# Kernel optimization log

Measured on AMD Instinct MI355X. Metric: run time of the kernel, lower is better.

Reference implementation:

```python
import jax, jax.numpy as jnp
import numpy as np

T, B, A = 128, 512, 5
X, Y, Z, H, R = 2, 10, 32, 128, 128
LOG2PI = np.float32(np.log(2.0 * np.pi))


def setup_inputs() -> dict:
    key = jax.random.key(0)
    ks = iter(jax.random.split(key, 40))
    w = lambda *s: jax.random.normal(next(ks), s, jnp.float32) * 0.05
    return dict(
        states=jax.random.normal(next(ks), (T, B, Y), jnp.float32),
        eps=jax.random.normal(next(ks), (T - 1, B, A, Z), jnp.float32),
        enc_w1=w(A, X + Y + R, H), enc_b1=w(A, H),
        enc_w2=w(A, H, H), enc_b2=w(A, H),
        enc_mw=w(A, H, Z), enc_mb=w(A, Z),
        enc_sw=w(A, H, Z), enc_sb=w(A, Z),
        pri_w1=w(A, Y + R, H), pri_b1=w(A, H),
        pri_w2=w(A, H, H), pri_b2=w(A, H),
        pri_mw=w(A, H, Z), pri_mb=w(A, Z),
        pri_sw=w(A, H, Z), pri_sb=w(A, Z),
        dec_w1=w(A, Y + Z + R, H), dec_b1=w(A, H),
        dec_w2=w(A, H, H), dec_b2=w(A, H),
        dec_mw=w(A, H, X), dec_mb=w(A, X),
        dec_sw=w(A, H, X), dec_sb=w(A, X),
        gru_wih=w(A, X + Z, 3 * R), gru_whh=w(A, R, 3 * R),
        gru_bih=w(A, 3 * R), gru_bhh=w(A, 3 * R),
    )


def _lin(x, wt, b):
    # x: [B, A, I], wt: [A, I, O] -> [B, A, O]  (per-agent linear)
    return jnp.einsum('bai,aio->bao', x, wt) + b


def _mlp(x, w1, b1, w2, b2):
    return jax.nn.relu(_lin(jax.nn.relu(_lin(x, w1, b1)), w2, b2))


def reference(states, eps, enc_w1, enc_b1, enc_w2, enc_b2, enc_mw, enc_mb,
              enc_sw, enc_sb, pri_w1, pri_b1, pri_w2, pri_b2, pri_mw, pri_mb,
              pri_sw, pri_sb, dec_w1, dec_b1, dec_w2, dec_b2, dec_mw, dec_mb,
              dec_sw, dec_sb, gru_wih, gru_whh, gru_bih, gru_bhh):
    y_all = states[:-1]                              # [T-1, B, Y]
    x_all = states[1:].reshape(T - 1, B, A, X)       # per-agent next positions

    def step(carry, xs):
        h, kl, nll = carry                           # h: [B, A, R]
        y, x, e = xs                                 # y:[B,Y] x:[B,A,X] e:[B,A,Z]
        yb = jnp.broadcast_to(y[:, None, :], (B, A, Y))
        enc_h = _mlp(jnp.concatenate([x, yb, h], -1), enc_w1, enc_b1, enc_w2, enc_b2)
        enc_m = _lin(enc_h, enc_mw, enc_mb)
        enc_s = jax.nn.softplus(_lin(enc_h, enc_sw, enc_sb))
        pri_h = _mlp(jnp.concatenate([yb, h], -1), pri_w1, pri_b1, pri_w2, pri_b2)
        pri_m = _lin(pri_h, pri_mw, pri_mb)
        pri_s = jax.nn.softplus(_lin(pri_h, pri_sw, pri_sb))
        z = enc_m + enc_s * e                         # reparameterized sample
        dec_h = _mlp(jnp.concatenate([yb, z, h], -1), dec_w1, dec_b1, dec_w2, dec_b2)
        dec_m = _lin(dec_h, dec_mw, dec_mb)
        dec_s = jax.nn.softplus(_lin(dec_h, dec_sw, dec_sb))
        # GRU cell (torch gate order: r, z, n)
        gi = _lin(jnp.concatenate([x, z], -1), gru_wih, gru_bih)   # [B,A,3R]
        gh = _lin(h, gru_whh, gru_bhh)
        gir, giz, gin = jnp.split(gi, 3, -1)
        ghr, ghz, ghn = jnp.split(gh, 3, -1)
        r = jax.nn.sigmoid(gir + ghr)
        u = jax.nn.sigmoid(giz + ghz)
        n = jnp.tanh(gin + r * ghn)
        h_new = (1.0 - u) * n + u * h
        kl_t = 0.5 * jnp.sum(2.0 * jnp.log(pri_s) - 2.0 * jnp.log(enc_s)
                             + (enc_s ** 2 + (enc_m - pri_m) ** 2) / pri_s ** 2 - 1.0)
        nll_t = jnp.sum(0.5 * LOG2PI + jnp.log(dec_s) + 0.5 * ((x - dec_m) / dec_s) ** 2)
        return (h_new, kl + kl_t, nll + nll_t), None

    h0 = jnp.zeros((B, A, R), states.dtype)
    zero = jnp.zeros((), states.dtype)
    (h, kl, nll), _ = jax.lax.scan(step, (h0, zero, zero), (y_all, x_all, eps))
    return jnp.stack([kl, nll])  # [kl_loss, recon_loss]
```

## Files before the change

kernel.cpp:

```cpp
#include <hip/hip_runtime.h>

typedef __attribute__((ext_vector_type(8))) short bf16x8;
typedef __attribute__((ext_vector_type(4))) float f32x4;

#define MFMA_B16(A,B,C) __builtin_amdgcn_mfma_f32_16x16x32_bf16((A),(B),(C),0,0,0)

#define FO_ENC1 0
#define FO_PRI1 48
#define FO_DEC1 88
#define FO_GIH  136
#define FO_GHH  184
#define FO_ENC2 280
#define FO_PRI2 312
#define FO_DEC2 344
#define FO_MS   376
#define FO_DECMS 408
#define NFRAG   412

#define MS 200
#define TS 136

__device__ __forceinline__ unsigned short f2bf(float f) {
  union { float f; unsigned u; } v; v.f = f;
  unsigned r = (v.u + 0x7fffu + ((v.u >> 16) & 1u)) >> 16;
  return (unsigned short)r;
}
__device__ __forceinline__ float bf2f(unsigned short h) {
  union { unsigned u; float f; } v; v.u = ((unsigned)h) << 16;
  return v.f;
}
__device__ __forceinline__ float sigm_(float x) { return 1.f / (1.f + __expf(-x)); }
__device__ __forceinline__ float tanh_(float x) {
  x = fminf(fmaxf(x, -15.f), 15.f);
  float e = __expf(-2.f * x);
  return (1.f - e) / (1.f + e);
}
__device__ __forceinline__ float splus_(float x) {
  return fmaxf(x, 0.f) + log1pf(__expf(-fabsf(x)));
}
__device__ __forceinline__ float ldnt(const float* p) {
  return __builtin_nontemporal_load(p);
}

__global__ void prep_kernel(const float* __restrict__ ew1, const float* __restrict__ pw1,
                            const float* __restrict__ dw1, const float* __restrict__ wih,
                            const float* __restrict__ whh, const float* __restrict__ ew2,
                            const float* __restrict__ pw2, const float* __restrict__ dw2,
                            const float* __restrict__ emw, const float* __restrict__ esw,
                            const float* __restrict__ pmw, const float* __restrict__ psw,
                            const float* __restrict__ dmw, const float* __restrict__ dsw,
                            unsigned short* __restrict__ ws)
{
  int blk = blockIdx.x;
  int a = blk / NFRAG, f = blk % NFRAG;
  int l = threadIdx.x, lg = l >> 4, ln = l & 15;
  float v[8];

  if (f < FO_PRI1) {
    int fi = f, nt = fi / 6, kb = fi % 6, n = nt * 16 + ln;
#pragma unroll
    for (int j = 0; j < 8; ++j) {
      int mk = kb * 32 + lg * 8 + j;
      int r = (mk < 2) ? mk : (mk >= 34 && mk < 44) ? 2 + (mk - 34)
            : (mk >= 64) ? 12 + (mk - 64) : -1;
      v[j] = (r >= 0) ? ew1[((size_t)a * 140 + r) * 128 + n] : 0.f;
    }
  } else if (f < FO_DEC1) {
    int fi = f - FO_PRI1, nt = fi / 5, kb = 1 + fi % 5, n = nt * 16 + ln;
#pragma unroll
    for (int j = 0; j < 8; ++j) {
      int mk = kb * 32 + lg * 8 + j;
      int r = (mk >= 34 && mk < 44) ? (mk - 34) : (mk >= 64) ? 10 + (mk - 64) : -1;
      v[j] = (r >= 0) ? pw1[((size_t)a * 138 + r) * 128 + n] : 0.f;
    }
  } else if (f < FO_GIH) {
    int fi = f - FO_DEC1, nt = fi / 6, kb = fi % 6, n = nt * 16 + ln;
#pragma unroll
    for (int j = 0; j < 8; ++j) {
      int mk = kb * 32 + lg * 8 + j;
      int r = (mk >= 2 && mk < 34) ? 10 + (mk - 2) : (mk >= 34 && mk < 44) ? (mk - 34)
            : (mk >= 64) ? 42 + (mk - 64) : -1;
      v[j] = (r >= 0) ? dw1[((size_t)a * 170 + r) * 128 + n] : 0.f;
    }
  } else if (f < FO_GHH) {
    int fi = f - FO_GIH, nt = fi / 2, kb = fi % 2, n = nt * 16 + ln;
#pragma unroll
    for (int j = 0; j < 8; ++j) {
      int mk = kb * 32 + lg * 8 + j;
      v[j] = (mk < 34) ? wih[((size_t)a * 34 + mk) * 384 + n] : 0.f;
    }
  } else if (f < FO_ENC2) {
    int fi = f - FO_GHH, nt = fi / 4, kb = fi % 4, n = nt * 16 + ln;
#pragma unroll
    for (int j = 0; j < 8; ++j) {
      int r = kb * 32 + lg * 8 + j;
      v[j] = whh[((size_t)a * 128 + r) * 384 + n];
    }
  } else if (f < FO_DEC2) {
    int fi = f - FO_ENC2;
    const float* W = (fi < 32) ? ew2 : pw2;
    fi &= 31;
    int nt = fi / 4, kb = fi % 4, n = nt * 16 + ln;
#pragma unroll
    for (int j = 0; j < 8; ++j) {
      int r = kb * 32 + lg * 8 + j;
      v[j] = W[((size_t)a * 128 + r) * 128 + n];
    }
  } else if (f < FO_MS) {
    int fi = f - FO_DEC2, nt = fi / 4, kb = fi % 4, n = nt * 16 + ln;
#pragma unroll
    for (int j = 0; j < 8; ++j) {
      int r = kb * 32 + lg * 8 + j;
      v[j] = dw2[((size_t)a * 128 + r) * 128 + n];
    }
  } else if (f < FO_DECMS) {
    int fi = f - FO_MS, mat = fi / 8, rem = fi % 8, nt = rem / 4, kb = rem % 4;
    int n = nt * 16 + ln;
    const float* W = (mat == 0) ? emw : (mat == 1) ? esw : (mat == 2) ? pmw : psw;
#pragma unroll
    for (int j = 0; j < 8; ++j) {
      int r = kb * 32 + lg * 8 + j;
      v[j] = W[((size_t)a * 128 + r) * 32 + n];
    }
  } else {
    int kb = f - FO_DECMS;
#pragma unroll
    for (int j = 0; j < 8; ++j) {
      int r = kb * 32 + lg * 8 + j;
      v[j] = (ln < 2) ? dmw[((size_t)a * 128 + r) * 2 + ln]
           : (ln < 4) ? dsw[((size_t)a * 128 + r) * 2 + (ln - 2)] : 0.f;
    }
  }
  unsigned short* dst = ws + (size_t)blk * 512 + l * 8;
#pragma unroll
  for (int j = 0; j < 8; ++j) dst[j] = f2bf(v[j]);
}

#define LD_FRAG(idx) (*(const bf16x8*)(fa + (size_t)(idx) * 512 + l * 8))

__global__ __launch_bounds__(256, 1) void vrnn_main(
    const float* __restrict__ states, const float* __restrict__ eps,
    const float* __restrict__ eb1, const float* __restrict__ eb2,
    const float* __restrict__ emb, const float* __restrict__ esb,
    const float* __restrict__ pb1, const float* __restrict__ pb2,
    const float* __restrict__ pmb, const float* __restrict__ psb,
    const float* __restrict__ db1, const float* __restrict__ db2,
    const float* __restrict__ dmb, const float* __restrict__ dsb,
    const float* __restrict__ bih, const float* __restrict__ bhh,
    const unsigned short* __restrict__ frags, float* __restrict__ out)
{
  const int a = blockIdx.y;
  const int b0 = blockIdx.x * 16;
  const int tid = threadIdx.x;
  const int w = tid >> 6, l = tid & 63, lg = l >> 4, ln = l & 15;

  __shared__ __align__(16) unsigned short ghh_lds[96 * 512];
  __shared__ __align__(16) unsigned short ms_lds[32 * 512];
  __shared__ __align__(16) unsigned short dms_lds[4 * 512];
  __shared__ __align__(16) unsigned short master[16 * MS];
  __shared__ __align__(16) unsigned short t1e[16 * TS], t1p[16 * TS];
  __shared__ __align__(16) unsigned short he[16 * TS], hp[16 * TS];
  __shared__ float msbuf[2][16][32];
  __shared__ float red[8];

  const unsigned short* fa = frags + (size_t)a * NFRAG * 512;

  {
    const uint4* s1 = (const uint4*)(fa + (size_t)FO_GHH * 512);
    uint4* d1 = (uint4*)ghh_lds;
    for (int i = tid; i < 96 * 64; i += 256) d1[i] = s1[i];
    const uint4* s2 = (const uint4*)(fa + (size_t)FO_MS * 512);
    uint4* d2 = (uint4*)ms_lds;
    for (int i = tid; i < 32 * 64; i += 256) d2[i] = s2[i];
    const uint4* s3 = (const uint4*)(fa + (size_t)FO_DECMS * 512);
    uint4* d3 = (uint4*)dms_lds;
    d3[tid] = s3[tid];
  }
  for (int i = tid; i < 16 * MS; i += 256) master[i] = 0;

  float eb1v[2], pb1v[2], eb2v[2], pb2v[2], db2v[2], d1b[2], ghb[3][2];
#pragma unroll
  for (int j = 0; j < 2; ++j) {
    int n = (w + 4 * j) * 16 + ln;
    eb1v[j] = eb1[a * 128 + n]; pb1v[j] = pb1[a * 128 + n];
    eb2v[j] = eb2[a * 128 + n]; pb2v[j] = pb2[a * 128 + n];
    db2v[j] = db2[a * 128 + n]; d1b[j]  = db1[a * 128 + n];
#pragma unroll
    for (int g = 0; g < 3; ++g)
      ghb[g][j] = bih[a * 384 + g * 128 + n] + bhh[a * 384 + g * 128 + n];
  }
  float hbm, hbs, dmsb = 0.f;
  if (w < 2) { hbm = emb[a * 32 + w * 16 + ln]; hbs = esb[a * 32 + w * 16 + ln]; }
  else { hbm = pmb[a * 32 + (w - 2) * 16 + ln]; hbs = psb[a * 32 + (w - 2) * 16 + ln]; }
  if (w == 0) dmsb = (ln < 2) ? dmb[a * 2 + ln] : (ln < 4) ? dsb[a * 2 + (ln - 2)] : 0.f;

  __syncthreads();

  if (tid < 160) {
    int row = tid / 10, c = tid - row * 10;
    master[row * MS + 34 + c] = f2bf(ldnt(states + (size_t)b0 * 10 + tid));
  }
  if (tid >= 192 && tid < 224) {
    int i = tid - 192, row = i >> 1, c = i & 1;
    master[row * MS + c] = f2bf(ldnt(states + ((size_t)512 + b0 + row) * 10 + a * 2 + c));
  }
  float e_cur[4] = {0.f, 0.f, 0.f, 0.f};
  if (w < 2) {
#pragma unroll
    for (int q = 0; q < 4; ++q)
      e_cur[q] = ldnt(eps + ((size_t)(b0 + 4 * lg + q) * 5 + a) * 32 + w * 16 + ln);
  }
  float xv[4] = {0.f, 0.f, 0.f, 0.f};
  float kl = 0.f, nll = 0.f;
  f32x4 em = {0, 0, 0, 0}, esv = {0, 0, 0, 0};
  f32x4 gh[3][2];
  float hn[8];
  __syncthreads();

  for (int t = 0; t < 127; ++t) {
    if (w == 0 && t > 0) {
      f32x4 acc = {dmsb, dmsb, dmsb, dmsb};
#pragma unroll
      for (int kb = 0; kb < 4; ++kb) {
        bf16x8 ad = *(const bf16x8*)&he[ln * TS + kb * 32 + lg * 8];
        bf16x8 bf = *(const bf16x8*)&dms_lds[kb * 512 + l * 8];
        acc = MFMA_B16(ad, bf, acc);
      }
#pragma unroll
      for (int q = 0; q < 4; ++q) {
        float sv = __shfl(splus_(acc[q]), l + 2);
        if (ln < 2) {
          float d = (xv[q] - acc[q]) / sv;
          nll += 0.9189385332f + __logf(sv) + 0.5f * d * d;
        }
      }
    }
    {
      bf16x8 f1[12], f2[10];
#pragma unroll
      for (int j = 0; j < 2; ++j) {
#pragma unroll
        for (int kb = 0; kb < 6; ++kb) f1[j * 6 + kb] = LD_FRAG(FO_ENC1 + (w + 4 * j) * 6 + kb);
#pragma unroll
        for (int kb = 0; kb < 5; ++kb) f2[j * 5 + kb] = LD_FRAG(FO_PRI1 + (w + 4 * j) * 5 + kb);
      }
      bf16x8 am[6];
#pragma unroll
      for (int kb = 0; kb < 6; ++kb)
        am[kb] = *(const bf16x8*)&master[ln * MS + kb * 32 + lg * 8];
#pragma unroll
      for (int j = 0; j < 2; ++j) {
        f32x4 a1 = {eb1v[j], eb1v[j], eb1v[j], eb1v[j]};
        f32x4 a2 = {pb1v[j], pb1v[j], pb1v[j], pb1v[j]};
#pragma unroll
        for (int kb = 0; kb < 6; ++kb) a1 = MFMA_B16(am[kb], f1[j * 6 + kb], a1);
#pragma unroll
        for (int kb = 0; kb < 5; ++kb) a2 = MFMA_B16(am[kb + 1], f2[j * 5 + kb], a2);
#pragma unroll
        for (int q = 0; q < 4; ++q) {
          t1e[(4 * lg + q) * TS + (w + 4 * j) * 16 + ln] = f2bf(fmaxf(a1[q], 0.f));
          t1p[(4 * lg + q) * TS + (w + 4 * j) * 16 + ln] = f2bf(fmaxf(a2[q], 0.f));
        }
      }
    }
    __syncthreads();

    {
      bf16x8 g1[8], g2[8];
#pragma unroll
      for (int j = 0; j < 2; ++j)
#pragma unroll
        for (int kb = 0; kb < 4; ++kb) {
          g1[j * 4 + kb] = LD_FRAG(FO_ENC2 + (w + 4 * j) * 4 + kb);
          g2[j * 4 + kb] = LD_FRAG(FO_PRI2 + (w + 4 * j) * 4 + kb);
        }
      bf16x8 ae[4], ap[4];
#pragma unroll
      for (int kb = 0; kb < 4; ++kb) {
        ae[kb] = *(const bf16x8*)&t1e[ln * TS + kb * 32 + lg * 8];
        ap[kb] = *(const bf16x8*)&t1p[ln * TS + kb * 32 + lg * 8];
      }
#pragma unroll
      for (int j = 0; j < 2; ++j) {
        f32x4 a1 = {eb2v[j], eb2v[j], eb2v[j], eb2v[j]};
        f32x4 a2 = {pb2v[j], pb2v[j], pb2v[j], pb2v[j]};
#pragma unroll
        for (int kb = 0; kb < 4; ++kb) {
          a1 = MFMA_B16(ae[kb], g1[j * 4 + kb], a1);
          a2 = MFMA_B16(ap[kb], g2[j * 4 + kb], a2);
        }
#pragma unroll
        for (int q = 0; q < 4; ++q) {
          he[(4 * lg + q) * TS + (w + 4 * j) * 16 + ln] = f2bf(fmaxf(a1[q], 0.f));
          hp[(4 * lg + q) * TS + (w + 4 * j) * 16 + ln] = f2bf(fmaxf(a2[q], 0.f));
        }
      }
    }
    __syncthreads();

    {
      const unsigned short* hs = (w < 2) ? he : hp;
      int mbase = ((w < 2) ? 0 : 16) + (w & 1) * 4;
      bf16x8 ah[4];
#pragma unroll
      for (int kb = 0; kb < 4; ++kb)
        ah[kb] = *(const bf16x8*)&hs[ln * TS + kb * 32 + lg * 8];
      f32x4 m = {hbm, hbm, hbm, hbm}, s = {hbs, hbs, hbs, hbs};
#pragma unroll
      for (int kb = 0; kb < 4; ++kb) {
        m = MFMA_B16(ah[kb], *(const bf16x8*)&ms_lds[(mbase + kb) * 512 + l * 8], m);
        s = MFMA_B16(ah[kb], *(const bf16x8*)&ms_lds[(mbase + 8 + kb) * 512 + l * 8], s);
      }
      if (w < 2) {
        em = m;
#pragma unroll
        for (int q = 0; q < 4; ++q) {
          esv[q] = splus_(s[q]);
          master[(4 * lg + q) * MS + 2 + w * 16 + ln] = f2bf(m[q] + esv[q] * e_cur[q]);
        }
      } else {
#pragma unroll
        for (int q = 0; q < 4; ++q) {
          msbuf[0][4 * lg + q][(w - 2) * 16 + ln] = m[q];
          msbuf[1][4 * lg + q][(w - 2) * 16 + ln] = splus_(s[q]);
        }
      }
      bf16x8 ahh[4];
#pragma unroll
      for (int kb = 0; kb < 4; ++kb)
        ahh[kb] = *(const bf16x8*)&master[ln * MS + (kb + 2) * 32 + lg * 8];
#pragma unroll
      for (int g = 0; g < 3; ++g)
#pragma unroll
        for (int j = 0; j < 2; ++j) {
          float bv = ghb[g][j];
          gh[g][j] = (f32x4){bv, bv, bv, bv};
        }
#pragma unroll
      for (int kb = 0; kb < 4; ++kb)
#pragma unroll
        for (int g = 0; g < 3; ++g)
#pragma unroll
          for (int j = 0; j < 2; ++j)
            gh[g][j] = MFMA_B16(ahh[kb],
              *(const bf16x8*)&ghh_lds[(size_t)((g * 8 + w + 4 * j) * 4 + kb) * 512 + l * 8],
              gh[g][j]);
    }
    __syncthreads();

    {
      if (w < 2 && t < 126) {
#pragma unroll
        for (int q = 0; q < 4; ++q)
          e_cur[q] = ldnt(eps + ((size_t)((t + 1) * 512 + b0 + 4 * lg + q) * 5 + a) * 32
                          + w * 16 + ln);
      }
      if (w == 0) {
#pragma unroll
        for (int q = 0; q < 4; ++q)
          xv[q] = ldnt(states + ((size_t)(t + 1) * 512 + b0 + 4 * lg + q) * 10
                       + a * 2 + (ln & 1));
      }
      bf16x8 fd[12], fg[12];
#pragma unroll
      for (int j = 0; j < 2; ++j)
#pragma unroll
        for (int kb = 0; kb < 6; ++kb)
          fd[j * 6 + kb] = LD_FRAG(FO_DEC1 + (w + 4 * j) * 6 + kb);
#pragma unroll
      for (int g = 0; g < 3; ++g)
#pragma unroll
        for (int j = 0; j < 2; ++j)
#pragma unroll
          for (int kb = 0; kb < 2; ++kb)
            fg[g * 4 + j * 2 + kb] = LD_FRAG(FO_GIH + (g * 8 + w + 4 * j) * 2 + kb);
      bf16x8 am[6];
#pragma unroll
      for (int kb = 0; kb < 6; ++kb)
        am[kb] = *(const bf16x8*)&master[ln * MS + kb * 32 + lg * 8];
#pragma unroll
      for (int j = 0; j < 2; ++j) {
        f32x4 acc = {d1b[j], d1b[j], d1b[j], d1b[j]};
#pragma unroll
        for (int kb = 0; kb < 6; ++kb) acc = MFMA_B16(am[kb], fd[j * 6 + kb], acc);
#pragma unroll
        for (int q = 0; q < 4; ++q)
          t1e[(4 * lg + q) * TS + (w + 4 * j) * 16 + ln] = f2bf(fmaxf(acc[q], 0.f));
      }
      f32x4 gi[3][2];
#pragma unroll
      for (int g = 0; g < 3; ++g)
#pragma unroll
        for (int j = 0; j < 2; ++j) gi[g][j] = (f32x4){0.f, 0.f, 0.f, 0.f};
#pragma unroll
      for (int kb = 0; kb < 2; ++kb)
#pragma unroll
        for (int g = 0; g < 3; ++g)
#pragma unroll
          for (int j = 0; j < 2; ++j)
            gi[g][j] = MFMA_B16(am[kb], fg[g * 4 + j * 2 + kb], gi[g][j]);
#pragma unroll
      for (int j = 0; j < 2; ++j)
#pragma unroll
        for (int q = 0; q < 4; ++q) {
          float r_ = sigm_(gi[0][j][q] + gh[0][j][q]);
          float u_ = sigm_(gi[1][j][q] + gh[1][j][q]);
          float n_ = tanh_(gi[2][j][q] + r_ * gh[2][j][q]);
          float ho = bf2f(master[(4 * lg + q) * MS + 64 + (w + 4 * j) * 16 + ln]);
          hn[j * 4 + q] = (1.f - u_) * n_ + u_ * ho;
        }
      if (w < 2) {
#pragma unroll
        for (int q = 0; q < 4; ++q) {
          float pm = msbuf[0][4 * lg + q][w * 16 + ln];
          float ps = msbuf[1][4 * lg + q][w * 16 + ln];
          float dm = em[q] - pm;
          float es2 = esv[q] * esv[q];
          kl += 0.5f * (2.f * __logf(ps) - 2.f * __logf(esv[q]) + (es2 + dm * dm) / (ps * ps) - 1.f);
        }
      }
    }
    __syncthreads();

    {
      bf16x8 fd2[8];
#pragma unroll
      for (int j = 0; j < 2; ++j)
#pragma unroll
        for (int kb = 0; kb < 4; ++kb)
          fd2[j * 4 + kb] = LD_FRAG(FO_DEC2 + (w + 4 * j) * 4 + kb);
      bf16x8 ad[4];
#pragma unroll
      for (int kb = 0; kb < 4; ++kb)
        ad[kb] = *(const bf16x8*)&t1e[ln * TS + kb * 32 + lg * 8];
#pragma unroll
      for (int j = 0; j < 2; ++j) {
        f32x4 acc = {db2v[j], db2v[j], db2v[j], db2v[j]};
#pragma unroll
        for (int kb = 0; kb < 4; ++kb) acc = MFMA_B16(ad[kb], fd2[j * 4 + kb], acc);
#pragma unroll
        for (int q = 0; q < 4; ++q)
          he[(4 * lg + q) * TS + (w + 4 * j) * 16 + ln] = f2bf(fmaxf(acc[q], 0.f));
      }
#pragma unroll
      for (int j = 0; j < 2; ++j)
#pragma unroll
        for (int q = 0; q < 4; ++q)
          master[(4 * lg + q) * MS + 64 + (w + 4 * j) * 16 + ln] = f2bf(hn[j * 4 + q]);
      if (t < 126) {
        if (w >= 1) {
          int i = (w - 1) * 64 + l;
          if (i < 160) {
            int row = i / 10, c = i - row * 10;
            master[row * MS + 34 + c] =
              f2bf(ldnt(states + ((size_t)(t + 1) * 512 + b0) * 10 + i));
          }
        }
        if (w == 0 && l < 32) {
          int row = l >> 1, c = l & 1;
          master[row * MS + c] =
            f2bf(ldnt(states + ((size_t)(t + 2) * 512 + b0 + row) * 10 + a * 2 + c));
        }
      }
    }
    __syncthreads();
  }

  if (w == 0) {
    f32x4 acc = {dmsb, dmsb, dmsb, dmsb};
#pragma unroll
    for (int kb = 0; kb < 4; ++kb) {
      bf16x8 ad = *(const bf16x8*)&he[ln * TS + kb * 32 + lg * 8];
      bf16x8 bf = *(const bf16x8*)&dms_lds[kb * 512 + l * 8];
      acc = MFMA_B16(ad, bf, acc);
    }
#pragma unroll
    for (int q = 0; q < 4; ++q) {
      float sv = __shfl(splus_(acc[q]), l + 2);
      if (ln < 2) {
        float d = (xv[q] - acc[q]) / sv;
        nll += 0.9189385332f + __logf(sv) + 0.5f * d * d;
      }
    }
  }

#pragma unroll
  for (int off = 32; off > 0; off >>= 1) {
    kl += __shfl_down(kl, off);
    nll += __shfl_down(nll, off);
  }
  if (l == 0) { red[w] = kl; red[4 + w] = nll; }
  __syncthreads();
  if (tid == 0) {
    float K = 0.f, N = 0.f;
#pragma unroll
    for (int i = 0; i < 4; ++i) { K += red[i]; N += red[4 + i]; }
    atomicAdd(out, K);
    atomicAdd(out + 1, N);
  }
}

extern "C" void kernel_launch(void* const* d_in, const int* in_sizes, int n_in,
                              void* d_out, int out_size, void* d_ws, size_t ws_size,
                              hipStream_t stream) {
  (void)in_sizes; (void)n_in; (void)out_size; (void)ws_size;
  const float* states = (const float*)d_in[0];
  const float* eps    = (const float*)d_in[1];
  const float* ew1 = (const float*)d_in[2];
  const float* eb1 = (const float*)d_in[3];
  const float* ew2 = (const float*)d_in[4];
  const float* eb2 = (const float*)d_in[5];
  const float* emw = (const float*)d_in[6];
  const float* emb = (const float*)d_in[7];
  const float* esw = (const float*)d_in[8];
  const float* esb = (const float*)d_in[9];
  const float* pw1 = (const float*)d_in[10];
  const float* pb1 = (const float*)d_in[11];
  const float* pw2 = (const float*)d_in[12];
  const float* pb2 = (const float*)d_in[13];
  const float* pmw = (const float*)d_in[14];
  const float* pmb = (const float*)d_in[15];
  const float* psw = (const float*)d_in[16];
  const float* psb = (const float*)d_in[17];
  const float* dw1 = (const float*)d_in[18];
  const float* db1 = (const float*)d_in[19];
  const float* dw2 = (const float*)d_in[20];
  const float* db2 = (const float*)d_in[21];
  const float* dmw = (const float*)d_in[22];
  const float* dmb = (const float*)d_in[23];
  const float* dsw = (const float*)d_in[24];
  const float* dsb = (const float*)d_in[25];
  const float* wih = (const float*)d_in[26];
  const float* whh = (const float*)d_in[27];
  const float* bih = (const float*)d_in[28];
  const float* bhh = (const float*)d_in[29];

  unsigned short* frags = (unsigned short*)d_ws;
  float* out = (float*)d_out;

  hipMemsetAsync(d_out, 0, 2 * sizeof(float), stream);
  prep_kernel<<<dim3(5 * NFRAG), dim3(64), 0, stream>>>(
      ew1, pw1, dw1, wih, whh, ew2, pw2, dw2, emw, esw, pmw, psw, dmw, dsw, frags);
  vrnn_main<<<dim3(32, 5), dim3(256), 0, stream>>>(
      states, eps, eb1, eb2, emb, esb, pb1, pb2, pmb, psb,
      db1, db2, dmb, dsb, bih, bhh, frags, out);
}
```

Measured before the change: 1.013 ms.

## Restructure VRNN step into three barrier phases with deferred decoder layer two

Reorganizes the per-timestep schedule from four barrier-separated phases to three. The decoder second layer and its mean/std head are deferred into the next step's phases, so they overlap with independent encoder/prior work. The GRU hidden-hidden matmul is hoisted into phase two, and the hidden state is kept in fp32 registers. The master input buffer is double-buffered (MS widened) so next-step states can be prefetched earlier, and mean/std head weights now come from global instead of LDS. The costs are more shared memory, extra buffers, and different LDS/global traffic per step.

```diff
diff --git a/kernel.cpp b/kernel.cpp
--- a/kernel.cpp
+++ b/kernel.cpp
@@ -17,7 +17,7 @@
 #define FO_DECMS 408
 #define NFRAG   412
 
-#define MS 200
+#define MS 264
 #define TS 136
 
 __device__ __forceinline__ unsigned short f2bf(float f) {
@@ -155,12 +155,12 @@
   const int w = tid >> 6, l = tid & 63, lg = l >> 4, ln = l & 15;
 
   __shared__ __align__(16) unsigned short ghh_lds[96 * 512];
-  __shared__ __align__(16) unsigned short ms_lds[32 * 512];
   __shared__ __align__(16) unsigned short dms_lds[4 * 512];
   __shared__ __align__(16) unsigned short master[16 * MS];
   __shared__ __align__(16) unsigned short t1e[16 * TS], t1p[16 * TS];
   __shared__ __align__(16) unsigned short he[16 * TS], hp[16 * TS];
-  __shared__ float msbuf[2][16][32];
+  __shared__ __align__(16) unsigned short t1d[16 * TS], hdbuf[16 * TS];
+  __shared__ float msbuf[4][16][32];
   __shared__ float red[8];
 
   const unsigned short* fa = frags + (size_t)a * NFRAG * 512;
@@ -169,9 +169,6 @@
     const uint4* s1 = (const uint4*)(fa + (size_t)FO_GHH * 512);
     uint4* d1 = (uint4*)ghh_lds;
     for (int i = tid; i < 96 * 64; i += 256) d1[i] = s1[i];
-    const uint4* s2 = (const uint4*)(fa + (size_t)FO_MS * 512);
-    uint4* d2 = (uint4*)ms_lds;
-    for (int i = tid; i < 32 * 64; i += 256) d2[i] = s2[i];
     const uint4* s3 = (const uint4*)(fa + (size_t)FO_DECMS * 512);
     uint4* d3 = (uint4*)dms_lds;
     d3[tid] = s3[tid];
@@ -198,7 +195,7 @@
 
   if (tid < 160) {
     int row = tid / 10, c = tid - row * 10;
-    master[row * MS + 34 + c] = f2bf(ldnt(states + (size_t)b0 * 10 + tid));
+    master[row * MS + 34 + c] = f2bf(ldnt(states + (size_t)(b0 + row) * 10 + c));
   }
   if (tid >= 192 && tid < 224) {
     int i = tid - 192, row = i >> 1, c = i & 1;
@@ -211,30 +208,26 @@
       e_cur[q] = ldnt(eps + ((size_t)(b0 + 4 * lg + q) * 5 + a) * 32 + w * 16 + ln);
   }
   float xv[4] = {0.f, 0.f, 0.f, 0.f};
+  float h_reg[2][4];
+#pragma unroll
+  for (int j = 0; j < 2; ++j)
+#pragma unroll
+    for (int q = 0; q < 4; ++q) h_reg[j][q] = 0.f;
   float kl = 0.f, nll = 0.f;
-  f32x4 em = {0, 0, 0, 0}, esv = {0, 0, 0, 0};
   f32x4 gh[3][2];
-  float hn[8];
   __syncthreads();
 
   for (int t = 0; t < 127; ++t) {
-    if (w == 0 && t > 0) {
-      f32x4 acc = {dmsb, dmsb, dmsb, dmsb};
-#pragma unroll
-      for (int kb = 0; kb < 4; ++kb) {
-        bf16x8 ad = *(const bf16x8*)&he[ln * TS + kb * 32 + lg * 8];
-        bf16x8 bf = *(const bf16x8*)&dms_lds[kb * 512 + l * 8];
-        acc = MFMA_B16(ad, bf, acc);
-      }
-#pragma unroll
-      for (int q = 0; q < 4; ++q) {
-        float sv = __shfl(splus_(acc[q]), l + 2);
-        if (ln < 2) {
-          float d = (xv[q] - acc[q]) / sv;
-          nll += 0.9189385332f + __logf(sv) + 0.5f * d * d;
-        }
-      }
-    }
+    const int base_t = (t & 1) * 200;
+    const int base_n = ((t + 1) & 1) * 200;
+
+    bf16x8 amA[2], am_h[4];
+#pragma unroll
+    for (int kb = 0; kb < 2; ++kb)
+      amA[kb] = *(const bf16x8*)&master[ln * MS + base_t + kb * 32 + lg * 8];
+#pragma unroll
+    for (int kb = 0; kb < 4; ++kb)
+      am_h[kb] = *(const bf16x8*)&master[ln * MS + 64 + kb * 32 + lg * 8];
     {
       bf16x8 f1[12], f2[10];
 #pragma unroll
@@ -244,18 +237,16 @@
 #pragma unroll
         for (int kb = 0; kb < 5; ++kb) f2[j * 5 + kb] = LD_FRAG(FO_PRI1 + (w + 4 * j) * 5 + kb);
       }
-      bf16x8 am[6];
-#pragma unroll
-      for (int kb = 0; kb < 6; ++kb)
-        am[kb] = *(const bf16x8*)&master[ln * MS + kb * 32 + lg * 8];
 #pragma unroll
       for (int j = 0; j < 2; ++j) {
         f32x4 a1 = {eb1v[j], eb1v[j], eb1v[j], eb1v[j]};
         f32x4 a2 = {pb1v[j], pb1v[j], pb1v[j], pb1v[j]};
 #pragma unroll
-        for (int kb = 0; kb < 6; ++kb) a1 = MFMA_B16(am[kb], f1[j * 6 + kb], a1);
-#pragma unroll
-        for (int kb = 0; kb < 5; ++kb) a2 = MFMA_B16(am[kb + 1], f2[j * 5 + kb], a2);
+        for (int kb = 0; kb < 6; ++kb)
+          a1 = MFMA_B16(kb < 2 ? amA[kb] : am_h[kb - 2], f1[j * 6 + kb], a1);
+#pragma unroll
+        for (int i = 0; i < 5; ++i)
+          a2 = MFMA_B16(i == 0 ? amA[1] : am_h[i - 1], f2[j * 5 + i], a2);
 #pragma unroll
         for (int q = 0; q < 4; ++q) {
           t1e[(4 * lg + q) * TS + (w + 4 * j) * 16 + ln] = f2bf(fmaxf(a1[q], 0.f));
@@ -295,12 +286,34 @@
           hp[(4 * lg + q) * TS + (w + 4 * j) * 16 + ln] = f2bf(fmaxf(a2[q], 0.f));
         }
       }
+#pragma unroll
+      for (int g = 0; g < 3; ++g)
+#pragma unroll
+        for (int j = 0; j < 2; ++j) {
+          float bv = ghb[g][j];
+          gh[g][j] = (f32x4){bv, bv, bv, bv};
+        }
+#pragma unroll
+      for (int kb = 0; kb < 4; ++kb)
+#pragma unroll
+        for (int g = 0; g < 3; ++g)
+#pragma unroll
+          for (int j = 0; j < 2; ++j)
+            gh[g][j] = MFMA_B16(am_h[kb],
+              *(const bf16x8*)&ghh_lds[(size_t)((g * 8 + w + 4 * j) * 4 + kb) * 512 + l * 8],
+              gh[g][j]);
     }
     __syncthreads();
 
     {
       const unsigned short* hs = (w < 2) ? he : hp;
-      int mbase = ((w < 2) ? 0 : 16) + (w & 1) * 4;
+      int mbase = FO_MS + ((w < 2) ? 0 : 16) + (w & 1) * 4;
+      bf16x8 fm[4], fs[4];
+#pragma unroll
+      for (int kb = 0; kb < 4; ++kb) {
+        fm[kb] = LD_FRAG(mbase + kb);
+        fs[kb] = LD_FRAG(mbase + 8 + kb);
+      }
       bf16x8 ah[4];
 #pragma unroll
       for (int kb = 0; kb < 4; ++kb)
@@ -308,53 +321,65 @@
       f32x4 m = {hbm, hbm, hbm, hbm}, s = {hbs, hbs, hbs, hbs};
 #pragma unroll
       for (int kb = 0; kb < 4; ++kb) {
-        m = MFMA_B16(ah[kb], *(const bf16x8*)&ms_lds[(mbase + kb) * 512 + l * 8], m);
-        s = MFMA_B16(ah[kb], *(const bf16x8*)&ms_lds[(mbase + 8 + kb) * 512 + l * 8], s);
+        m = MFMA_B16(ah[kb], fm[kb], m);
+        s = MFMA_B16(ah[kb], fs[kb], s);
       }
       if (w < 2) {
-        em = m;
 #pragma unroll
         for (int q = 0; q < 4; ++q) {
-          esv[q] = splus_(s[q]);
-          master[(4 * lg + q) * MS + 2 + w * 16 + ln] = f2bf(m[q] + esv[q] * e_cur[q]);
+          float es = splus_(s[q]);
+          msbuf[0][4 * lg + q][w * 16 + ln] = m[q];
+          msbuf[1][4 * lg + q][w * 16 + ln] = es;
+          master[(4 * lg + q) * MS + base_t + 2 + w * 16 + ln] = f2bf(m[q] + es * e_cur[q]);
         }
       } else {
 #pragma unroll
         for (int q = 0; q < 4; ++q) {
-          msbuf[0][4 * lg + q][(w - 2) * 16 + ln] = m[q];
-          msbuf[1][4 * lg + q][(w - 2) * 16 + ln] = splus_(s[q]);
-        }
-      }
-      bf16x8 ahh[4];
-#pragma unroll
-      for (int kb = 0; kb < 4; ++kb)
-        ahh[kb] = *(const bf16x8*)&master[ln * MS + (kb + 2) * 32 + lg * 8];
-#pragma unroll
-      for (int g = 0; g < 3; ++g)
+          msbuf[2][4 * lg + q][(w - 2) * 16 + ln] = m[q];
+          msbuf[3][4 * lg + q][(w - 2) * 16 + ln] = splus_(s[q]);
+        }
+      }
+      if (t > 0) {
+        bf16x8 fd2[8];
+#pragma unroll
+        for (int j = 0; j < 2; ++j)
+#pragma unroll
+          for (int kb = 0; kb < 4; ++kb)
+            fd2[j * 4 + kb] = LD_FRAG(FO_DEC2 + (w + 4 * j) * 4 + kb);
+        bf16x8 ad[4];
+#pragma unroll
+        for (int kb = 0; kb < 4; ++kb)
+          ad[kb] = *(const bf16x8*)&t1d[ln * TS + kb * 32 + lg * 8];
 #pragma unroll
         for (int j = 0; j < 2; ++j) {
-          float bv = ghb[g][j];
-          gh[g][j] = (f32x4){bv, bv, bv, bv};
-        }
-#pragma unroll
-      for (int kb = 0; kb < 4; ++kb)
-#pragma unroll
-        for (int g = 0; g < 3; ++g)
-#pragma unroll
-          for (int j = 0; j < 2; ++j)
-            gh[g][j] = MFMA_B16(ahh[kb],
-              *(const bf16x8*)&ghh_lds[(size_t)((g * 8 + w + 4 * j) * 4 + kb) * 512 + l * 8],
-              gh[g][j]);
+          f32x4 acc = {db2v[j], db2v[j], db2v[j], db2v[j]};
+#pragma unroll
+          for (int kb = 0; kb < 4; ++kb) acc = MFMA_B16(ad[kb], fd2[j * 4 + kb], acc);
+#pragma unroll
+          for (int q = 0; q < 4; ++q)
+            hdbuf[(4 * lg + q) * TS + (w + 4 * j) * 16 + ln] = f2bf(fmaxf(acc[q], 0.f));
+        }
+      }
+      if (t < 126) {
+        if (tid < 160) {
+          int row = tid / 10, c = tid - row * 10;
+          master[row * MS + base_n + 34 + c] =
+            f2bf(ldnt(states + ((size_t)(t + 1) * 512 + b0 + row) * 10 + c));
+        }
+        if (tid >= 192 && tid < 224) {
+          int i = tid - 192, row = i >> 1, c = i & 1;
+          master[row * MS + base_n + c] =
+            f2bf(ldnt(states + ((size_t)(t + 2) * 512 + b0 + row) * 10 + a * 2 + c));
+        }
+      }
     }
     __syncthreads();
 
     {
-      if (w < 2 && t < 126) {
-#pragma unroll
-        for (int q = 0; q < 4; ++q)
-          e_cur[q] = ldnt(eps + ((size_t)((t + 1) * 512 + b0 + 4 * lg + q) * 5 + a) * 32
-                          + w * 16 + ln);
-      }
+      bf16x8 amZ[2];
+#pragma unroll
+      for (int kb = 0; kb < 2; ++kb)
+        amZ[kb] = *(const bf16x8*)&master[ln * MS + base_t + kb * 32 + lg * 8];
       if (w == 0) {
 #pragma unroll
         for (int q = 0; q < 4; ++q)
@@ -374,18 +399,34 @@
 #pragma unroll
           for (int kb = 0; kb < 2; ++kb)
             fg[g * 4 + j * 2 + kb] = LD_FRAG(FO_GIH + (g * 8 + w + 4 * j) * 2 + kb);
-      bf16x8 am[6];
-#pragma unroll
-      for (int kb = 0; kb < 6; ++kb)
-        am[kb] = *(const bf16x8*)&master[ln * MS + kb * 32 + lg * 8];
+
+      if (w == 0 && t > 0) {
+        f32x4 acc = {dmsb, dmsb, dmsb, dmsb};
+#pragma unroll
+        for (int kb = 0; kb < 4; ++kb) {
+          bf16x8 ad = *(const bf16x8*)&hdbuf[ln * TS + kb * 32 + lg * 8];
+          bf16x8 bf = *(const bf16x8*)&dms_lds[kb * 512 + l * 8];
+          acc = MFMA_B16(ad, bf, acc);
+        }
+#pragma unroll
+        for (int q = 0; q < 4; ++q) {
+          float sv = __shfl(splus_(acc[q]), l + 2);
+          if (ln < 2) {
+            float d = (xv[q] - acc[q]) / sv;
+            nll += 0.9189385332f + __logf(sv) + 0.5f * d * d;
+          }
+        }
+      }
+
 #pragma unroll
       for (int j = 0; j < 2; ++j) {
         f32x4 acc = {d1b[j], d1b[j], d1b[j], d1b[j]};
 #pragma unroll
-        for (int kb = 0; kb < 6; ++kb) acc = MFMA_B16(am[kb], fd[j * 6 + kb], acc);
+        for (int kb = 0; kb < 6; ++kb)
+          acc = MFMA_B16(kb < 2 ? amZ[kb] : am_h[kb - 2], fd[j * 6 + kb], acc);
 #pragma unroll
         for (int q = 0; q < 4; ++q)
-          t1e[(4 * lg + q) * TS + (w + 4 * j) * 16 + ln] = f2bf(fmaxf(acc[q], 0.f));
+          t1d[(4 * lg + q) * TS + (w + 4 * j) * 16 + ln] = f2bf(fmaxf(acc[q], 0.f));
       }
       f32x4 gi[3][2];
 #pragma unroll
@@ -398,7 +439,7 @@
         for (int g = 0; g < 3; ++g)
 #pragma unroll
           for (int j = 0; j < 2; ++j)
-            gi[g][j] = MFMA_B16(am[kb], fg[g * 4 + j * 2 + kb], gi[g][j]);
+            gi[g][j] = MFMA_B16(amZ[kb], fg[g * 4 + j * 2 + kb], gi[g][j]);
 #pragma unroll
       for (int j = 0; j < 2; ++j)
 #pragma unroll
@@ -406,71 +447,57 @@
           float r_ = sigm_(gi[0][j][q] + gh[0][j][q]);
           float u_ = sigm_(gi[1][j][q] + gh[1][j][q]);
           float n_ = tanh_(gi[2][j][q] + r_ * gh[2][j][q]);
-          float ho = bf2f(master[(4 * lg + q) * MS + 64 + (w + 4 * j) * 16 + ln]);
-          hn[j * 4 + q] = (1.f - u_) * n_ + u_ * ho;
-        }
-      if (w < 2) {
-#pragma unroll
-        for (int q = 0; q < 4; ++q) {
-          float pm = msbuf[0][4 * lg + q][w * 16 + ln];
-          float ps = msbuf[1][4 * lg + q][w * 16 + ln];
-          float dm = em[q] - pm;
-          float es2 = esv[q] * esv[q];
-          kl += 0.5f * (2.f * __logf(ps) - 2.f * __logf(esv[q]) + (es2 + dm * dm) / (ps * ps) - 1.f);
-        }
+          float hn = (1.f - u_) * n_ + u_ * h_reg[j][q];
+          h_reg[j][q] = hn;
+          master[(4 * lg + q) * MS + 64 + (w + 4 * j) * 16 + ln] = f2bf(hn);
+        }
+#pragma unroll
+      for (int rr = 0; rr < 2; ++rr) {
+        int elem = rr * 64 + l;
+        int row = w * 4 + (elem >> 5), col = elem & 31;
+        float em_ = msbuf[0][row][col], es_ = msbuf[1][row][col];
+        float pm_ = msbuf[2][row][col], ps_ = msbuf[3][row][col];
+        float dm = em_ - pm_;
+        kl += 0.5f * (2.f * __logf(ps_) - 2.f * __logf(es_)
+                      + (es_ * es_ + dm * dm) / (ps_ * ps_) - 1.f);
+      }
+      if (w < 2 && t < 126) {
+#pragma unroll
+        for (int q = 0; q < 4; ++q)
+          e_cur[q] = ldnt(eps + ((size_t)((t + 1) * 512 + b0 + 4 * lg + q) * 5 + a) * 32
+                          + w * 16 + ln);
       }
     }
     __syncthreads();
-
-    {
-      bf16x8 fd2[8];
-#pragma unroll
-      for (int j = 0; j < 2; ++j)
-#pragma unroll
-        for (int kb = 0; kb < 4; ++kb)
-          fd2[j * 4 + kb] = LD_FRAG(FO_DEC2 + (w + 4 * j) * 4 + kb);
-      bf16x8 ad[4];
+  }
+
+  {
+    bf16x8 fd2[8];
+#pragma unroll
+    for (int j = 0; j < 2; ++j)
 #pragma unroll
       for (int kb = 0; kb < 4; ++kb)
-        ad[kb] = *(const bf16x8*)&t1e[ln * TS + kb * 32 + lg * 8];
-#pragma unroll
-      for (int j = 0; j < 2; ++j) {
-        f32x4 acc = {db2v[j], db2v[j], db2v[j], db2v[j]};
-#pragma unroll
-        for (int kb = 0; kb < 4; ++kb) acc = MFMA_B16(ad[kb], fd2[j * 4 + kb], acc);
-#pragma unroll
-        for (int q = 0; q < 4; ++q)
-          he[(4 * lg + q) * TS + (w + 4 * j) * 16 + ln] = f2bf(fmaxf(acc[q], 0.f));
-      }
-#pragma unroll
-      for (int j = 0; j < 2; ++j)
-#pragma unroll
-        for (int q = 0; q < 4; ++q)
-          master[(4 * lg + q) * MS + 64 + (w + 4 * j) * 16 + ln] = f2bf(hn[j * 4 + q]);
-      if (t < 126) {
-        if (w >= 1) {
-          int i = (w - 1) * 64 + l;
-          if (i < 160) {
-            int row = i / 10, c = i - row * 10;
-            master[row * MS + 34 + c] =
-              f2bf(ldnt(states + ((size_t)(t + 1) * 512 + b0) * 10 + i));
-          }
-        }
-        if (w == 0 && l < 32) {
-          int row = l >> 1, c = l & 1;
-          master[row * MS + c] =
-            f2bf(ldnt(states + ((size_t)(t + 2) * 512 + b0 + row) * 10 + a * 2 + c));
-        }
-      }
-    }
-    __syncthreads();
-  }
-
+        fd2[j * 4 + kb] = LD_FRAG(FO_DEC2 + (w + 4 * j) * 4 + kb);
+    bf16x8 ad[4];
+#pragma unroll
+    for (int kb = 0; kb < 4; ++kb)
+      ad[kb] = *(const bf16x8*)&t1d[ln * TS + kb * 32 + lg * 8];
+#pragma unroll
+    for (int j = 0; j < 2; ++j) {
+      f32x4 acc = {db2v[j], db2v[j], db2v[j], db2v[j]};
+#pragma unroll
+      for (int kb = 0; kb < 4; ++kb) acc = MFMA_B16(ad[kb], fd2[j * 4 + kb], acc);
+#pragma unroll
+      for (int q = 0; q < 4; ++q)
+        hdbuf[(4 * lg + q) * TS + (w + 4 * j) * 16 + ln] = f2bf(fmaxf(acc[q], 0.f));
+    }
+  }
+  __syncthreads();
   if (w == 0) {
     f32x4 acc = {dmsb, dmsb, dmsb, dmsb};
 #pragma unroll
     for (int kb = 0; kb < 4; ++kb) {
-      bf16x8 ad = *(const bf16x8*)&he[ln * TS + kb * 32 + lg * 8];
+      bf16x8 ad = *(const bf16x8*)&hdbuf[ln * TS + kb * 32 + lg * 8];
       bf16x8 bf = *(const bf16x8*)&dms_lds[kb * 512 + l * 8];
       acc = MFMA_B16(ad, bf, acc);
     }
```

Result: faster. 976.8 us (-3.6%).
